# Kernel tuning notes

Hardware: AMD Instinct MI355X
Metric: run time of the kernel (lower is better)

Reference implementation:

```python
import jax, jax.numpy as jnp
import numpy as np

N = 2048   # num_params = feature dim = number of ring Givens angles
B = 16384  # batch


def setup_inputs() -> dict:
    key = jax.random.key(0)
    k1, k2 = jax.random.split(key)
    x = jax.random.normal(k1, (B, N), dtype=jnp.float32)
    angles = jax.random.normal(k2, (N,), dtype=jnp.float32)
    return {"x": x, "angles": angles}


def _build_rotation(angles):
    """R = G_0 @ G_1 @ ... @ G_{n-1}, built by sequential right-multiplication.

    Right-multiplying M by Givens G_k (plane (i, j)=(k, (k+1)%n), angle theta_k,
    with G[i,i]=c, G[j,i]=s, G[i,j]=-s, G[j,j]=c) only mixes columns i and j:
        new_col_i =  c*col_i + s*col_j
        new_col_j = -s*col_i + c*col_j
    This is O(n) per step -> O(n^2) total, identical math to the original
    O(n^4) loop of full n x n matmuls against per-step identity matrices.
    """
    n = angles.shape[0]
    idx_i = jnp.arange(n)
    idx_j = (idx_i + 1) % n

    def step(M, inp):
        theta, i, j = inp
        c = jnp.cos(theta)
        s = jnp.sin(theta)
        col_i = M[:, i]
        col_j = M[:, j]
        M = M.at[:, i].set(c * col_i + s * col_j)
        M = M.at[:, j].set(-s * col_i + c * col_j)
        return M, None

    M0 = jnp.eye(n, dtype=angles.dtype)
    R, _ = jax.lax.scan(step, M0, (angles, idx_i, idx_j))
    return R


def reference(x, angles):
    R = _build_rotation(angles)   # [N, N], orthogonal (product of Givens)
    return x @ R.T                # [B, N]
```

## Files before the change

### kernel.cpp

```cpp
#include <hip/hip_runtime.h>
#include <stdint.h>

#define NN  2048
#define QPS 8
#define QPR 512
#define WPB 4
#define RPW 8

#define GLOBAL_AS __attribute__((address_space(1)))
#define LDS_AS    __attribute__((address_space(3)))

__global__ __launch_bounds__(256, 2) void ring_givens_scan_kernel(
        const float* __restrict__ x,
        const float* __restrict__ angles,
        float* __restrict__ y,
        int B) {
    __shared__ float4 buf[WPB][2][QPR];
    const int lane = threadIdx.x & 63;
    const int wib  = threadIdx.x >> 6;
    float4* b0 = buf[wib][0];
    float4* b1 = buf[wib][1];

    float4 A[QPS], Bq[QPS];
    {
        const float4* ap4 = (const float4*)(angles + lane * 32);
        #pragma unroll
        for (int q = 0; q < QPS; ++q) {
            float4 av = ap4[q];
            float ss, cc;
            sincosf(av.x, &ss, &cc); A[q].x = cc;  A[q].y = ss;
            sincosf(av.y, &ss, &cc); A[q].z = cc;  A[q].w = ss;
            sincosf(av.z, &ss, &cc); Bq[q].x = cc; Bq[q].y = ss;
            sincosf(av.w, &ss, &cc); Bq[q].z = cc; Bq[q].w = ss;
        }
    }
    float sl, cl;
    sincosf(angles[NN - 1], &sl, &cl);

    float Mseg = 1.0f;
    #pragma unroll
    for (int q = 0; q < QPS; ++q)
        Mseg *= (A[q].y * A[q].w) * (Bq[q].y * Bq[q].w);
    float Ms[6];
    float Mc = Mseg;
    #pragma unroll
    for (int d = 1, st = 0; d < 64; d <<= 1, ++st) {
        Ms[st] = (lane + d < 64) ? Mc : 0.0f;
        float Mo = __shfl_down(Mc, d);
        if (lane + d < 64) Mc = Mc * Mo;
    }
    float Mn = __shfl_down(Mc, 1);
    Mn = (lane == 63) ? 1.0f : Mn;

    const int gwid        = blockIdx.x * WPB + wib;
    const int total_waves = gridDim.x * WPB;

    if (gwid < B) {
        const float4* xr4 = (const float4*)(x + (size_t)gwid * NN);
        #pragma unroll
        for (int t = 0; t < 8; ++t) {
            const int srcq = (t * 64 + lane) ^ ((lane >> 3) & 7);
            __builtin_amdgcn_global_load_lds(
                (const GLOBAL_AS uint32_t*)(const void*)(xr4 + srcq),
                (LDS_AS uint32_t*)(void*)(b0 + t * 64), 16, 0, 0);
        }
    }

    for (int r = 0; r < RPW; ++r) {
        const int row = gwid + r * total_waves;
        if (row >= B) break;
        float4* P = (r & 1) ? b1 : b0;
        float4* Q = (r & 1) ? b0 : b1;

        if (r == 0) asm volatile("s_waitcnt vmcnt(0)" ::: "memory");
        else        asm volatile("s_waitcnt vmcnt(8)" ::: "memory");

        const int nrow = row + total_waves;
        if (r + 1 < RPW && nrow < B) {
            const float4* xn4 = (const float4*)(x + (size_t)nrow * NN);
            #pragma unroll
            for (int t = 0; t < 8; ++t) {
                const int srcq = (t * 64 + lane) ^ ((lane >> 3) & 7);
                __builtin_amdgcn_global_load_lds(
                    (const GLOBAL_AS uint32_t*)(const void*)(xn4 + srcq),
                    (LDS_AS uint32_t*)(void*)(Q + t * 64), 16, 0, 0);
            }
        }

        const int segq = lane * QPS;
        float4 w4[QPS];
        #pragma unroll
        for (int q = 0; q < QPS; ++q)
            w4[q] = P[segq + (q ^ (lane & 7))];

        const float x0v = __shfl(w4[0].x, 0);
        const float xlv = __shfl(w4[7].w, 63);
        const float t0  = sl * xlv + cl * x0v;
        if (lane == 0) w4[0].x = t0;

        float U = 0.0f;
        #pragma unroll
        for (int q = QPS - 1; q >= 0; --q) {
            U = Bq[q].z * w4[q].w - Bq[q].w * U;
            U = Bq[q].x * w4[q].z - Bq[q].y * U;
            U = A[q].z  * w4[q].y - A[q].w  * U;
            U = A[q].x  * w4[q].x - A[q].y  * U;
        }

        #pragma unroll
        for (int d = 1, st = 0; d < 64; d <<= 1, ++st) {
            float Uo = __shfl_down(U, d);
            U = fmaf(Ms[st], Uo, U);
        }
        float Un = __shfl_down(U, 1);
        Un = (lane == 63) ? 0.0f : Un;
        float a = fmaf(Mn, x0v, Un);

        float e31, p0, p1, p2;
        {
            float4 v = w4[7];
            e31 = Bq[7].w * v.w + Bq[7].z * a;  a = Bq[7].z * v.w - Bq[7].w * a;
            p2  = Bq[7].y * v.z + Bq[7].x * a;  a = Bq[7].x * v.z - Bq[7].y * a;
            p1  = A[7].w  * v.y + A[7].z  * a;  a = A[7].z  * v.y - A[7].w  * a;
            p0  = A[7].y  * v.x + A[7].x  * a;  a = A[7].x  * v.x - A[7].y  * a;
        }
        #pragma unroll
        for (int q = QPS - 2; q >= 0; --q) {
            float4 v = w4[q];
            float e3 = Bq[q].w * v.w + Bq[q].z * a;  a = Bq[q].z * v.w - Bq[q].w * a;
            P[segq + ((q + 1) ^ (lane & 7))] = make_float4(e3, p0, p1, p2);
            float e2 = Bq[q].y * v.z + Bq[q].x * a;  a = Bq[q].x * v.z - Bq[q].y * a;
            float e1 = A[q].w  * v.y + A[q].z  * a;  a = A[q].z  * v.y - A[q].w  * a;
            float e0 = A[q].y  * v.x + A[q].x  * a;  a = A[q].x  * v.x - A[q].y  * a;
            p0 = e0; p1 = e1; p2 = e2;
        }
        float prev = __shfl_up(e31, 1);
        float s0v  = (lane == 0) ? a : prev;
        P[segq + (0 ^ (lane & 7))] = make_float4(s0v, p0, p1, p2);

        float4* __restrict__ yr4 = (float4*)(y + (size_t)row * NN);
        #pragma unroll
        for (int t = 0; t < 8; ++t) {
            const int p = t * 64 + lane;
            float4 v = P[p ^ ((lane >> 3) & 7)];
            yr4[p] = v;
        }
    }
}

extern "C" void kernel_launch(void* const* d_in, const int* in_sizes, int n_in,
                              void* d_out, int out_size, void* d_ws, size_t ws_size,
                              hipStream_t stream) {
    const float* x      = (const float*)d_in[0];
    const float* angles = (const float*)d_in[1];
    float* y            = (float*)d_out;

    const int B = in_sizes[0] / NN;
    const int total_waves = (B + RPW - 1) / RPW;
    const int blocks = (total_waves + WPB - 1) / WPB;
    hipLaunchKernelGGL(ring_givens_scan_kernel, dim3(blocks), dim3(256), 0, stream,
                       x, angles, y, B);
}
```

Before: 238.2 us.

## Process two rows per wave with direct register loads and nontemporal stores

Replaces the async global-to-LDS double-buffered input prefetch with per-lane contiguous register loads, and interleaves two independent rows per iteration so the serial Givens recurrences and shuffle scans of both rows overlap. LDS is now used only to transpose outputs before coalesced stores, and the stores use nontemporal hints. Input loads become strided per lane (each lane reads 128 contiguous bytes), which may hurt coalescing, and register pressure roughly doubles. Out-of-range rows are clamped rather than skipped.

```diff
diff --git a/kernel.cpp b/kernel.cpp
--- a/kernel.cpp
+++ b/kernel.cpp
@@ -7,27 +7,25 @@
 #define WPB 4
 #define RPW 8
 
-#define GLOBAL_AS __attribute__((address_space(1)))
-#define LDS_AS    __attribute__((address_space(3)))
+typedef float f32x4 __attribute__((ext_vector_type(4)));
 
 __global__ __launch_bounds__(256, 2) void ring_givens_scan_kernel(
         const float* __restrict__ x,
         const float* __restrict__ angles,
         float* __restrict__ y,
         int B) {
-    __shared__ float4 buf[WPB][2][QPR];
+    __shared__ float4 obuf[WPB][2][QPR];
     const int lane = threadIdx.x & 63;
     const int wib  = threadIdx.x >> 6;
-    float4* b0 = buf[wib][0];
-    float4* b1 = buf[wib][1];
+    float4* const oA = obuf[wib][0];
+    float4* const oB = obuf[wib][1];
 
     float4 A[QPS], Bq[QPS];
     {
         const float4* ap4 = (const float4*)(angles + lane * 32);
         #pragma unroll
         for (int q = 0; q < QPS; ++q) {
-            float4 av = ap4[q];
-            float ss, cc;
+            float4 av = ap4[q]; float ss, cc;
             sincosf(av.x, &ss, &cc); A[q].x = cc;  A[q].y = ss;
             sincosf(av.y, &ss, &cc); A[q].z = cc;  A[q].w = ss;
             sincosf(av.z, &ss, &cc); Bq[q].x = cc; Bq[q].y = ss;
@@ -39,111 +37,135 @@
 
     float Mseg = 1.0f;
     #pragma unroll
-    for (int q = 0; q < QPS; ++q)
-        Mseg *= (A[q].y * A[q].w) * (Bq[q].y * Bq[q].w);
-    float Ms[6];
-    float Mc = Mseg;
+    for (int q = 0; q < QPS; ++q) Mseg *= (A[q].y * A[q].w) * (Bq[q].y * Bq[q].w);
+    float Ms[6]; float Mc = Mseg;
     #pragma unroll
     for (int d = 1, st = 0; d < 64; d <<= 1, ++st) {
         Ms[st] = (lane + d < 64) ? Mc : 0.0f;
         float Mo = __shfl_down(Mc, d);
-        if (lane + d < 64) Mc = Mc * Mo;
+        if (lane + d < 64) Mc *= Mo;
     }
     float Mn = __shfl_down(Mc, 1);
     Mn = (lane == 63) ? 1.0f : Mn;
 
-    const int gwid        = blockIdx.x * WPB + wib;
-    const int total_waves = gridDim.x * WPB;
+    const int TW   = gridDim.x * WPB;
+    const int gwid = blockIdx.x * WPB + wib;
 
-    if (gwid < B) {
-        const float4* xr4 = (const float4*)(x + (size_t)gwid * NN);
+    float4 wAr[QPS], wBr[QPS];
+    {
+        const int rA = min(gwid, B - 1);
+        const int rB = min(gwid + TW, B - 1);
+        const float4* xa = (const float4*)(x + (size_t)rA * NN) + lane * QPS;
+        const float4* xb = (const float4*)(x + (size_t)rB * NN) + lane * QPS;
         #pragma unroll
-        for (int t = 0; t < 8; ++t) {
-            const int srcq = (t * 64 + lane) ^ ((lane >> 3) & 7);
-            __builtin_amdgcn_global_load_lds(
-                (const GLOBAL_AS uint32_t*)(const void*)(xr4 + srcq),
-                (LDS_AS uint32_t*)(void*)(b0 + t * 64), 16, 0, 0);
-        }
+        for (int q = 0; q < QPS; ++q) { wAr[q] = xa[q]; wBr[q] = xb[q]; }
     }
 
-    for (int r = 0; r < RPW; ++r) {
-        const int row = gwid + r * total_waves;
-        if (row >= B) break;
-        float4* P = (r & 1) ? b1 : b0;
-        float4* Q = (r & 1) ? b0 : b1;
+    #pragma unroll
+    for (int p = 0; p < RPW / 2; ++p) {
+        const int rA = gwid + (2 * p) * TW;
+        const int rB = rA + TW;
 
-        if (r == 0) asm volatile("s_waitcnt vmcnt(0)" ::: "memory");
-        else        asm volatile("s_waitcnt vmcnt(8)" ::: "memory");
-
-        const int nrow = row + total_waves;
-        if (r + 1 < RPW && nrow < B) {
-            const float4* xn4 = (const float4*)(x + (size_t)nrow * NN);
-            #pragma unroll
-            for (int t = 0; t < 8; ++t) {
-                const int srcq = (t * 64 + lane) ^ ((lane >> 3) & 7);
-                __builtin_amdgcn_global_load_lds(
-                    (const GLOBAL_AS uint32_t*)(const void*)(xn4 + srcq),
-                    (LDS_AS uint32_t*)(void*)(Q + t * 64), 16, 0, 0);
-            }
+        const float x0A = __shfl(wAr[0].x, 0);
+        const float xlA = __shfl(wAr[7].w, 63);
+        const float x0B = __shfl(wBr[0].x, 0);
+        const float xlB = __shfl(wBr[7].w, 63);
+        if (lane == 0) {
+            wAr[0].x = sl * xlA + cl * x0A;
+            wBr[0].x = sl * xlB + cl * x0B;
         }
 
-        const int segq = lane * QPS;
-        float4 w4[QPS];
-        #pragma unroll
-        for (int q = 0; q < QPS; ++q)
-            w4[q] = P[segq + (q ^ (lane & 7))];
-
-        const float x0v = __shfl(w4[0].x, 0);
-        const float xlv = __shfl(w4[7].w, 63);
-        const float t0  = sl * xlv + cl * x0v;
-        if (lane == 0) w4[0].x = t0;
-
-        float U = 0.0f;
+        float UA = 0.0f, UB = 0.0f;
         #pragma unroll
         for (int q = QPS - 1; q >= 0; --q) {
-            U = Bq[q].z * w4[q].w - Bq[q].w * U;
-            U = Bq[q].x * w4[q].z - Bq[q].y * U;
-            U = A[q].z  * w4[q].y - A[q].w  * U;
-            U = A[q].x  * w4[q].x - A[q].y  * U;
+            UA = fmaf(-Bq[q].w, UA, Bq[q].z * wAr[q].w);
+            UB = fmaf(-Bq[q].w, UB, Bq[q].z * wBr[q].w);
+            UA = fmaf(-Bq[q].y, UA, Bq[q].x * wAr[q].z);
+            UB = fmaf(-Bq[q].y, UB, Bq[q].x * wBr[q].z);
+            UA = fmaf(-A[q].w,  UA, A[q].z  * wAr[q].y);
+            UB = fmaf(-A[q].w,  UB, A[q].z  * wBr[q].y);
+            UA = fmaf(-A[q].y,  UA, A[q].x  * wAr[q].x);
+            UB = fmaf(-A[q].y,  UB, A[q].x  * wBr[q].x);
         }
 
         #pragma unroll
         for (int d = 1, st = 0; d < 64; d <<= 1, ++st) {
-            float Uo = __shfl_down(U, d);
-            U = fmaf(Ms[st], Uo, U);
+            float UoA = __shfl_down(UA, d);
+            float UoB = __shfl_down(UB, d);
+            UA = fmaf(Ms[st], UoA, UA);
+            UB = fmaf(Ms[st], UoB, UB);
         }
-        float Un = __shfl_down(U, 1);
-        Un = (lane == 63) ? 0.0f : Un;
-        float a = fmaf(Mn, x0v, Un);
+        float UnA = __shfl_down(UA, 1);
+        float UnB = __shfl_down(UB, 1);
+        UnA = (lane == 63) ? 0.0f : UnA;
+        UnB = (lane == 63) ? 0.0f : UnB;
+        float aA = fmaf(Mn, x0A, UnA);
+        float aB = fmaf(Mn, x0B, UnB);
 
-        float e31, p0, p1, p2;
+        const int segq = lane * QPS;
+        float eA31, pA0, pA1, pA2, eB31, pB0, pB1, pB2;
         {
-            float4 v = w4[7];
-            e31 = Bq[7].w * v.w + Bq[7].z * a;  a = Bq[7].z * v.w - Bq[7].w * a;
-            p2  = Bq[7].y * v.z + Bq[7].x * a;  a = Bq[7].x * v.z - Bq[7].y * a;
-            p1  = A[7].w  * v.y + A[7].z  * a;  a = A[7].z  * v.y - A[7].w  * a;
-            p0  = A[7].y  * v.x + A[7].x  * a;  a = A[7].x  * v.x - A[7].y  * a;
+            float4 vA = wAr[7], vB = wBr[7];
+            eA31 = fmaf(Bq[7].z, aA, Bq[7].w * vA.w);  aA = fmaf(-Bq[7].w, aA, Bq[7].z * vA.w);
+            eB31 = fmaf(Bq[7].z, aB, Bq[7].w * vB.w);  aB = fmaf(-Bq[7].w, aB, Bq[7].z * vB.w);
+            pA2  = fmaf(Bq[7].x, aA, Bq[7].y * vA.z);  aA = fmaf(-Bq[7].y, aA, Bq[7].x * vA.z);
+            pB2  = fmaf(Bq[7].x, aB, Bq[7].y * vB.z);  aB = fmaf(-Bq[7].y, aB, Bq[7].x * vB.z);
+            pA1  = fmaf(A[7].z,  aA, A[7].w  * vA.y);  aA = fmaf(-A[7].w,  aA, A[7].z  * vA.y);
+            pB1  = fmaf(A[7].z,  aB, A[7].w  * vB.y);  aB = fmaf(-A[7].w,  aB, A[7].z  * vB.y);
+            pA0  = fmaf(A[7].x,  aA, A[7].y  * vA.x);  aA = fmaf(-A[7].y,  aA, A[7].x  * vA.x);
+            pB0  = fmaf(A[7].x,  aB, A[7].y  * vB.x);  aB = fmaf(-A[7].y,  aB, A[7].x  * vB.x);
         }
         #pragma unroll
         for (int q = QPS - 2; q >= 0; --q) {
-            float4 v = w4[q];
-            float e3 = Bq[q].w * v.w + Bq[q].z * a;  a = Bq[q].z * v.w - Bq[q].w * a;
-            P[segq + ((q + 1) ^ (lane & 7))] = make_float4(e3, p0, p1, p2);
-            float e2 = Bq[q].y * v.z + Bq[q].x * a;  a = Bq[q].x * v.z - Bq[q].y * a;
-            float e1 = A[q].w  * v.y + A[q].z  * a;  a = A[q].z  * v.y - A[q].w  * a;
-            float e0 = A[q].y  * v.x + A[q].x  * a;  a = A[q].x  * v.x - A[q].y  * a;
-            p0 = e0; p1 = e1; p2 = e2;
+            float4 vA = wAr[q], vB = wBr[q];
+            float eA3 = fmaf(Bq[q].z, aA, Bq[q].w * vA.w);  aA = fmaf(-Bq[q].w, aA, Bq[q].z * vA.w);
+            float eB3 = fmaf(Bq[q].z, aB, Bq[q].w * vB.w);  aB = fmaf(-Bq[q].w, aB, Bq[q].z * vB.w);
+            oA[segq + ((q + 1) ^ (lane & 7))] = make_float4(eA3, pA0, pA1, pA2);
+            oB[segq + ((q + 1) ^ (lane & 7))] = make_float4(eB3, pB0, pB1, pB2);
+            float eA2 = fmaf(Bq[q].x, aA, Bq[q].y * vA.z);  aA = fmaf(-Bq[q].y, aA, Bq[q].x * vA.z);
+            float eB2 = fmaf(Bq[q].x, aB, Bq[q].y * vB.z);  aB = fmaf(-Bq[q].y, aB, Bq[q].x * vB.z);
+            float eA1 = fmaf(A[q].z,  aA, A[q].w * vA.y);   aA = fmaf(-A[q].w,  aA, A[q].z * vA.y);
+            float eB1 = fmaf(A[q].z,  aB, A[q].w * vB.y);   aB = fmaf(-A[q].w,  aB, A[q].z * vB.y);
+            float eA0 = fmaf(A[q].x,  aA, A[q].y * vA.x);   aA = fmaf(-A[q].y,  aA, A[q].x * vA.x);
+            float eB0 = fmaf(A[q].x,  aB, A[q].y * vB.x);   aB = fmaf(-A[q].y,  aB, A[q].x * vB.x);
+            pA0 = eA0; pA1 = eA1; pA2 = eA2;
+            pB0 = eB0; pB1 = eB1; pB2 = eB2;
         }
-        float prev = __shfl_up(e31, 1);
-        float s0v  = (lane == 0) ? a : prev;
-        P[segq + (0 ^ (lane & 7))] = make_float4(s0v, p0, p1, p2);
+        {
+            float prevA = __shfl_up(eA31, 1);
+            float prevB = __shfl_up(eB31, 1);
+            float s0A = (lane == 0) ? aA : prevA;
+            float s0B = (lane == 0) ? aB : prevB;
+            oA[segq + (0 ^ (lane & 7))] = make_float4(s0A, pA0, pA1, pA2);
+            oB[segq + (0 ^ (lane & 7))] = make_float4(s0B, pB0, pB1, pB2);
+        }
 
-        float4* __restrict__ yr4 = (float4*)(y + (size_t)row * NN);
-        #pragma unroll
-        for (int t = 0; t < 8; ++t) {
-            const int p = t * 64 + lane;
-            float4 v = P[p ^ ((lane >> 3) & 7)];
-            yr4[p] = v;
+        if (p + 1 < RPW / 2) {
+            const int nA = min(rA + 2 * TW, B - 1);
+            const int nB = min(rB + 2 * TW, B - 1);
+            const float4* xa = (const float4*)(x + (size_t)nA * NN) + lane * QPS;
+            const float4* xb = (const float4*)(x + (size_t)nB * NN) + lane * QPS;
+            #pragma unroll
+            for (int q = 0; q < QPS; ++q) { wAr[q] = xa[q]; wBr[q] = xb[q]; }
+        }
+
+        if (rA < B) {
+            float4* yA4 = (float4*)(y + (size_t)rA * NN);
+            #pragma unroll
+            for (int t = 0; t < 8; ++t) {
+                const int pp = t * 64 + lane;
+                float4 v = oA[pp ^ ((lane >> 3) & 7)];
+                __builtin_nontemporal_store(*(const f32x4*)&v, (f32x4*)(yA4 + pp));
+            }
+        }
+        if (rB < B) {
+            float4* yB4 = (float4*)(y + (size_t)rB * NN);
+            #pragma unroll
+            for (int t = 0; t < 8; ++t) {
+                const int pp = t * 64 + lane;
+                float4 v = oB[pp ^ ((lane >> 3) & 7)];
+                __builtin_nontemporal_store(*(const f32x4*)&v, (f32x4*)(yB4 + pp));
+            }
         }
     }
 }
```

After: 243.9 us. 2.4% more time.
